# Performance work log

Hardware: AMD Instinct MI355X
Metric: run time of the kernel (lower is better)

## Reference

```python
import jax, jax.numpy as jnp
import numpy as np

B, N, DIM = 32, 577, 768   # N = num_patches + 1
H, DH = 12, 64             # heads, dim_head; inner_dim = H*DH = 768
NEG = -987654321.0         # LSA diagonal mask value from the source


def setup_inputs() -> dict:
    key = jax.random.key(0)
    ks = jax.random.split(key, 5)
    inner = H * DH
    base_scale = DH ** -0.5
    return {
        "x": jax.random.normal(ks[0], (B, N, DIM), dtype=jnp.float32),
        "W_qkv": jax.random.normal(ks[1], (DIM, inner * 3), dtype=jnp.float32) * (DIM ** -0.5),
        "scale": base_scale * (1.0 + 0.01 * jax.random.normal(ks[2], (H,), dtype=jnp.float32)),
        "W_out": jax.random.normal(ks[3], (inner, DIM), dtype=jnp.float32) * (inner ** -0.5),
        "b_out": jnp.zeros((DIM,), dtype=jnp.float32),
    }


def reference(x, W_qkv, scale, W_out, b_out):
    b, n, _ = x.shape
    qkv = x @ W_qkv                                   # [b, n, 3*H*DH]
    q, k, v = jnp.split(qkv, 3, axis=-1)
    to_heads = lambda t: t.reshape(b, n, H, DH).transpose(0, 2, 1, 3)  # b h n d
    q, k, v = to_heads(q), to_heads(k), to_heads(v)
    # per-head learnable scale (LSA)
    dots = jnp.einsum('bhid,bhjd->bhij', q, k) * scale[None, :, None, None]
    # mask self-attention diagonal (eye scatter in the torch source)
    eye = jnp.eye(n, dtype=bool)
    dots = jnp.where(eye[None, None], NEG, dots)
    attn = jax.nn.softmax(dots, axis=-1)
    out = jnp.einsum('bhij,bhjd->bhid', attn, v)      # b h n d
    out = out.transpose(0, 2, 1, 3).reshape(b, n, H * DH)
    return out @ W_out + b_out
```

## Files before the change

kernel.cpp:

```cpp
#include <hip/hip_runtime.h>


typedef _Float16 half8  __attribute__((ext_vector_type(8)));
typedef _Float16 h4f    __attribute__((ext_vector_type(4)));
typedef __fp16   hv2    __attribute__((ext_vector_type(2)));
typedef __fp16   hv4    __attribute__((ext_vector_type(4)));
typedef float    floatx4 __attribute__((ext_vector_type(4)));

#define MTOT   18464
#define NEG_V  (-987654321.0f)
#define VTS    584

__device__ __forceinline__ void gl_lds16(const _Float16* g, _Float16* l) {
    __builtin_amdgcn_global_load_lds(
        (const __attribute__((address_space(1))) unsigned int*)g,
        (__attribute__((address_space(3))) unsigned int*)l,
        16, 0, 0);
}

__global__ __launch_bounds__(256) void cvt_x(const float* __restrict__ x,
                                             _Float16* __restrict__ x16) {
    const size_t idx = ((size_t)blockIdx.x * 256 + threadIdx.x) * 8;
    half8 h = {};
    if (idx < (size_t)MTOT * 768) {
        float4 a = *(const float4*)(x + idx);
        float4 b = *(const float4*)(x + idx + 4);
        h[0] = (_Float16)a.x; h[1] = (_Float16)a.y;
        h[2] = (_Float16)a.z; h[3] = (_Float16)a.w;
        h[4] = (_Float16)b.x; h[5] = (_Float16)b.y;
        h[6] = (_Float16)b.z; h[7] = (_Float16)b.w;
    }
    *(half8*)(x16 + idx) = h;
}

__global__ __launch_bounds__(256) void transpose_w(const float* __restrict__ src,
                                                   _Float16* __restrict__ dst,
                                                   int K, int Ncol) {
    __shared__ float tile[32][33];
    const int n0 = blockIdx.x * 32, k0 = blockIdx.y * 32;
    const int tx = threadIdx.x & 31, ty = threadIdx.x >> 5;
    for (int i = 0; i < 32; i += 8)
        tile[ty + i][tx] = src[(size_t)(k0 + ty + i) * Ncol + (n0 + tx)];
    __syncthreads();
    for (int i = 0; i < 32; i += 8)
        dst[(size_t)(n0 + ty + i) * K + (k0 + tx)] = (_Float16)tile[tx][ty + i];
}

__global__ __launch_bounds__(512, 4) void gemm_qkv(const _Float16* __restrict__ x16,
                                                   const _Float16* __restrict__ wT,
                                                   const float* __restrict__ scale,
                                                   _Float16* __restrict__ qg,
                                                   _Float16* __restrict__ kg,
                                                   _Float16* __restrict__ vT) {
    __shared__ _Float16 As[2][128 * 32];
    __shared__ _Float16 Bs[2][256 * 32];
    const int m0 = blockIdx.x * 128, n0 = blockIdx.y * 256;
    const int tid = threadIdx.x;
    const int lane = tid & 63, wv = tid >> 6;
    const int wrow = wv >> 2, wcol = wv & 3;
    const int lr = lane & 15, lq = lane >> 4;

    const int ra  = tid >> 2,            ca  = (tid & 3) * 8;
    const int rb0 = tid >> 2,            cb0 = (tid & 3) * 8;
    const int rb1 = (512 + tid) >> 2,    cb1 = (tid & 3) * 8;

    floatx4 acc[4][4];
    const floatx4 fz = {0.f, 0.f, 0.f, 0.f};
    for (int i = 0; i < 4; ++i)
        for (int j = 0; j < 4; ++j) acc[i][j] = fz;

    #define STAGE_QKV(ki, bf)                                                     \
        do {                                                                      \
            const int kk_ = (ki) * 32;                                            \
            gl_lds16(x16 + (size_t)(m0 + ra) * 768 + kk_ + ca, &As[bf][wv*64*8]); \
            gl_lds16(wT + (size_t)(n0 + rb0) * 768 + kk_ + cb0, &Bs[bf][wv*64*8]);\
            gl_lds16(wT + (size_t)(n0 + rb1) * 768 + kk_ + cb1,                   \
                     &Bs[bf][(512 + wv*64) * 8]);                                 \
        } while (0)

    STAGE_QKV(0, 0);
    for (int ki = 0; ki < 24; ++ki) {
        const int bf = ki & 1;
        if (ki < 23) {
            STAGE_QKV(ki + 1, bf ^ 1);
            asm volatile("s_waitcnt vmcnt(3)" ::: "memory");
        } else {
            asm volatile("s_waitcnt vmcnt(0)" ::: "memory");
        }
        asm volatile("s_barrier" ::: "memory");

        half8 af[4], bfr[4];
        #pragma unroll
        for (int i = 0; i < 4; ++i)
            af[i] = *(const half8*)&As[bf][(wrow * 64 + i * 16 + lr) * 32 + lq * 8];
        #pragma unroll
        for (int j = 0; j < 4; ++j)
            bfr[j] = *(const half8*)&Bs[bf][(wcol * 64 + j * 16 + lr) * 32 + lq * 8];
        #pragma unroll
        for (int i = 0; i < 4; ++i)
            #pragma unroll
            for (int j = 0; j < 4; ++j)
                acc[i][j] = __builtin_amdgcn_mfma_f32_16x16x32_f16(af[i], bfr[j], acc[i][j], 0, 0, 0);

        asm volatile("s_waitcnt lgkmcnt(0)\n\ts_barrier" ::: "memory");
    }
    #undef STAGE_QKV

    const int cbase = n0 + wcol * 64;
    const int which = cbase / 768;
    const int h = (cbase - which * 768) >> 6;
    const float qsc = (which == 0) ? scale[h] * 1.4426950408889634f : 1.0f;
    #pragma unroll
    for (int j = 0; j < 4; ++j) {
        const int d = j * 16 + lr;
        #pragma unroll
        for (int i = 0; i < 4; ++i)
            #pragma unroll
            for (int r = 0; r < 4; ++r) {
                const int row = m0 + wrow * 64 + i * 16 + lq * 4 + r;
                if (row >= MTOT) continue;
                const unsigned bb = (unsigned)row / 577u;
                const unsigned nn = (unsigned)row - bb * 577u;
                const _Float16 val = (_Float16)(acc[i][j][r] * qsc);
                const size_t head = (size_t)(bb * 12 + h);
                if (which == 0)      qg[(head * 577 + nn) * 64 + d] = val;
                else if (which == 1) kg[(head * 577 + nn) * 64 + d] = val;
                else                 vT[(head * 64 + d) * VTS + nn] = val;
            }
    }
}

__global__ __launch_bounds__(256) void attn_kernel(const _Float16* __restrict__ qg,
                                                   const _Float16* __restrict__ kg,
                                                   const _Float16* __restrict__ vT,
                                                   _Float16* __restrict__ Og) {
    __shared__ __align__(16) _Float16 Ks[64 * 64];
    __shared__ __align__(16) _Float16 Vs[64 * 64];
    const int qt = blockIdx.x, h = blockIdx.y, b = blockIdx.z;
    const int tid = threadIdx.x, lane = tid & 63, wv = tid >> 6;
    const int lr = lane & 15, lq = lane >> 4;
    const size_t head = (size_t)(b * 12 + h);
    const _Float16* qh = qg + head * 577 * 64;
    const _Float16* kh = kg + head * 577 * 64;
    const _Float16* vh = vT + head * 64 * VTS;
    const int q0 = qt * 128;
    const int xs = lq ^ (lr & 7), xs4 = xs ^ 4;

    half8 bq[2][2];
    #pragma unroll
    for (int st = 0; st < 2; ++st) {
        const int qi = q0 + st * 64 + wv * 16 + lr;
        const int qc = qi < 577 ? qi : 576;
        bq[st][0] = *(const half8*)(qh + (size_t)qc * 64 + lq * 8);
        bq[st][1] = *(const half8*)(qh + (size_t)qc * 64 + 32 + lq * 8);
    }

    const floatx4 fz = {0.f, 0.f, 0.f, 0.f};
    floatx4 ot[2][4];
    #pragma unroll
    for (int st = 0; st < 2; ++st)
        #pragma unroll
        for (int c = 0; c < 4; ++c) ot[st][c] = fz;
    float sacc[2] = {0.f, 0.f};

    for (int kt = 0; kt < 10; ++kt) {
        const int j0 = kt * 64;
        __syncthreads();
        #pragma unroll
        for (int t = 0; t < 2; ++t) {
            const int c = t * 256 + wv * 64 + lane;
            const int row = c >> 3, cl = (c & 7) ^ (row & 7);
            gl_lds16(kh + (size_t)(j0 + row) * 64 + cl * 8,
                     Ks + (t * 256 + wv * 64) * 8);
            gl_lds16(vh + (size_t)row * VTS + j0 + cl * 8,
                     Vs + (t * 256 + wv * 64) * 8);
        }
        __syncthreads();

        half8 ak[4][2];
        #pragma unroll
        for (int ct = 0; ct < 4; ++ct) {
            const int base = (ct * 16 + lr) * 64;
            ak[ct][0] = *(const half8*)&Ks[base + xs * 8];
            ak[ct][1] = *(const half8*)&Ks[base + xs4 * 8];
        }

        floatx4 s[2][4];
        #pragma unroll
        for (int st = 0; st < 2; ++st)
            #pragma unroll
            for (int ct = 0; ct < 4; ++ct) {
                floatx4 t = __builtin_amdgcn_mfma_f32_16x16x32_f16(ak[ct][0], bq[st][0], fz, 0, 0, 0);
                s[st][ct] = __builtin_amdgcn_mfma_f32_16x16x32_f16(ak[ct][1], bq[st][1], t, 0, 0, 0);
            }

        if (kt == 9) {
            #pragma unroll
            for (int st = 0; st < 2; ++st) {
                s[st][0][0] = (lq == 0) ? s[st][0][0] : -INFINITY;
                s[st][0][1] = -INFINITY; s[st][0][2] = -INFINITY; s[st][0][3] = -INFINITY;
                #pragma unroll
                for (int ct = 1; ct < 4; ++ct) {
                    s[st][ct][0] = -INFINITY; s[st][ct][1] = -INFINITY;
                    s[st][ct][2] = -INFINITY; s[st][ct][3] = -INFINITY;
                }
            }
        }
        #pragma unroll
        for (int st = 0; st < 2; ++st) {
            if (kt == qt * 2 + st) {
                #pragma unroll
                for (int ct = 0; ct < 4; ++ct)
                    if (ct == wv) {
                        #pragma unroll
                        for (int r = 0; r < 4; ++r)
                            if (lq * 4 + r == lr) s[st][ct][r] = -INFINITY;
                    }
            }
        }

        hv4 pk[2][4];
        #pragma unroll
        for (int st = 0; st < 2; ++st)
            #pragma unroll
            for (int ct = 0; ct < 4; ++ct) {
                const float p0 = __builtin_amdgcn_exp2f(s[st][ct][0]);
                const float p1 = __builtin_amdgcn_exp2f(s[st][ct][1]);
                const float p2 = __builtin_amdgcn_exp2f(s[st][ct][2]);
                const float p3 = __builtin_amdgcn_exp2f(s[st][ct][3]);
                sacc[st] += (p0 + p1) + (p2 + p3);
                const hv2 lo = __builtin_amdgcn_cvt_pkrtz(p0, p1);
                const hv2 hi = __builtin_amdgcn_cvt_pkrtz(p2, p3);
                pk[st][ct] = __builtin_shufflevector(lo, hi, 0, 1, 2, 3);
            }

        #pragma unroll
        for (int jc = 0; jc < 4; ++jc) {
            const int csv = ((jc << 1) | (lq >> 1)) ^ (lr & 7);
            #pragma unroll
            for (int ctd = 0; ctd < 4; ++ctd) {
                const hv4 av = *(const hv4*)&Vs[(ctd * 16 + lr) * 64 + csv * 8 + (lq & 1) * 4];
                #pragma unroll
                for (int st = 0; st < 2; ++st)
                    ot[st][ctd] = __builtin_amdgcn_mfma_f32_16x16x16f16(av, pk[st][jc], ot[st][ctd], 0, 0, 0);
            }
        }
    }

    #pragma unroll
    for (int st = 0; st < 2; ++st) {
        float l = sacc[st];
        l += __shfl_xor(l, 16, 64);
        l += __shfl_xor(l, 32, 64);
        const float linv = 1.f / l;
        const int i = q0 + st * 64 + wv * 16 + lr;
        if (i < 577) {
            #pragma unroll
            for (int ctd = 0; ctd < 4; ++ctd) {
                h4f ov;
                #pragma unroll
                for (int r = 0; r < 4; ++r) ov[r] = (_Float16)(ot[st][ctd][r] * linv);
                *(h4f*)(Og + ((size_t)(b * 577 + i)) * 768 + h * 64 + ctd * 16 + lq * 4) = ov;
            }
        }
    }
}

__global__ __launch_bounds__(512, 4) void gemm_out(const _Float16* __restrict__ Og,
                                                   const _Float16* __restrict__ wT,
                                                   const float* __restrict__ bias,
                                                   float* __restrict__ out) {
    __shared__ _Float16 As[2][128 * 32];
    __shared__ _Float16 Bs[2][256 * 32];
    const int m0 = blockIdx.x * 128, n0 = blockIdx.y * 256;
    const int tid = threadIdx.x;
    const int lane = tid & 63, wv = tid >> 6;
    const int wrow = wv >> 2, wcol = wv & 3;
    const int lr = lane & 15, lq = lane >> 4;

    const int ra  = tid >> 2,         ca  = (tid & 3) * 8;
    const int rb0 = tid >> 2,         cb0 = (tid & 3) * 8;
    const int rb1 = (512 + tid) >> 2, cb1 = (tid & 3) * 8;

    floatx4 acc[4][4];
    const floatx4 fz = {0.f, 0.f, 0.f, 0.f};
    for (int i = 0; i < 4; ++i)
        for (int j = 0; j < 4; ++j) acc[i][j] = fz;

    #define STAGE_OUT(ki, bf)                                                     \
        do {                                                                      \
            const int kk_ = (ki) * 32;                                            \
            gl_lds16(Og + (size_t)(m0 + ra) * 768 + kk_ + ca, &As[bf][wv*64*8]);  \
            gl_lds16(wT + (size_t)(n0 + rb0) * 768 + kk_ + cb0, &Bs[bf][wv*64*8]);\
            gl_lds16(wT + (size_t)(n0 + rb1) * 768 + kk_ + cb1,                   \
                     &Bs[bf][(512 + wv*64) * 8]);                                 \
        } while (0)

    STAGE_OUT(0, 0);
    for (int ki = 0; ki < 24; ++ki) {
        const int bf = ki & 1;
        if (ki < 23) {
            STAGE_OUT(ki + 1, bf ^ 1);
            asm volatile("s_waitcnt vmcnt(3)" ::: "memory");
        } else {
            asm volatile("s_waitcnt vmcnt(0)" ::: "memory");
        }
        asm volatile("s_barrier" ::: "memory");

        half8 af[4], bfr[4];
        #pragma unroll
        for (int i = 0; i < 4; ++i)
            af[i] = *(const half8*)&As[bf][(wrow * 64 + i * 16 + lr) * 32 + lq * 8];
        #pragma unroll
        for (int j = 0; j < 4; ++j)
            bfr[j] = *(const half8*)&Bs[bf][(wcol * 64 + j * 16 + lr) * 32 + lq * 8];
        #pragma unroll
        for (int i = 0; i < 4; ++i)
            #pragma unroll
            for (int j = 0; j < 4; ++j)
                acc[i][j] = __builtin_amdgcn_mfma_f32_16x16x32_f16(af[i], bfr[j], acc[i][j], 0, 0, 0);

        asm volatile("s_waitcnt lgkmcnt(0)\n\ts_barrier" ::: "memory");
    }
    #undef STAGE_OUT

    #pragma unroll
    for (int j = 0; j < 4; ++j) {
        const int c = n0 + wcol * 64 + j * 16 + lr;
        const float bv = bias[c];
        #pragma unroll
        for (int i = 0; i < 4; ++i)
            #pragma unroll
            for (int r = 0; r < 4; ++r) {
                const int row = m0 + wrow * 64 + i * 16 + lq * 4 + r;
                if (row < MTOT) out[(size_t)row * 768 + c] = acc[i][j][r] + bv;
            }
    }
}

extern "C" void kernel_launch(void* const* d_in, const int* in_sizes, int n_in,
                              void* d_out, int out_size, void* d_ws, size_t ws_size,
                              hipStream_t stream) {
    const float* x      = (const float*)d_in[0];
    const float* W_qkv  = (const float*)d_in[1];
    const float* scale  = (const float*)d_in[2];
    const float* W_out  = (const float*)d_in[3];
    const float* b_out  = (const float*)d_in[4];
    float* out = (float*)d_out;

    char* ws = (char*)d_ws;
    _Float16* x16   = (_Float16*)(ws);
    _Float16* Og    = x16;
    _Float16* qg    = (_Float16*)(ws + 28508160u);
    _Float16* kg    = (_Float16*)(ws + 28508160u + 28360704u);
    _Float16* vT    = (_Float16*)(ws + 28508160u + 2u * 28360704u);
    _Float16* WqkvT = (_Float16*)(ws + 28508160u + 2u * 28360704u + 28704768u);
    _Float16* WoutT = WqkvT + (size_t)2304 * 768;

    cvt_x<<<6960, 256, 0, stream>>>(x, x16);
    transpose_w<<<dim3(72, 24), 256, 0, stream>>>(W_qkv, WqkvT, 768, 2304);
    transpose_w<<<dim3(24, 24), 256, 0, stream>>>(W_out, WoutT, 768, 768);
    gemm_qkv<<<dim3(145, 9), 512, 0, stream>>>(x16, WqkvT, scale, qg, kg, vT);
    attn_kernel<<<dim3(5, 12, 32), 256, 0, stream>>>(qg, kg, vT, Og);
    gemm_out<<<dim3(145, 3), 512, 0, stream>>>(Og, WoutT, b_out, out);
}
```

Baseline: 352.1 us.

## Deepen GEMM pipelines to six LDS stages, swizzle tiles, double-buffer attention K/V

Both projection GEMMs now use a 6-slot LDS ring with loads issued four k-steps ahead, and drop the trailing barrier because the ring distance keeps reuse safe. LDS tile columns are XOR-swizzled to reduce bank conflicts, and s_setprio brackets the MFMA blocks. The attention kernel double-buffers K/V tiles so the next tile's loads overlap the current compute. The larger LDS footprint lowers the occupancy target to 2 blocks per CU, which trades latency hiding from extra resident waves for deeper prefetch.

After: 404.1 us. 14.8% more time.

```diff
diff --git a/kernel.cpp b/kernel.cpp
--- a/kernel.cpp
+++ b/kernel.cpp
@@ -46,43 +46,51 @@
         dst[(size_t)(n0 + ty + i) * K + (k0 + tx)] = (_Float16)tile[tx][ty + i];
 }
 
-__global__ __launch_bounds__(512, 4) void gemm_qkv(const _Float16* __restrict__ x16,
+__global__ __launch_bounds__(512, 2) void gemm_qkv(const _Float16* __restrict__ x16,
                                                    const _Float16* __restrict__ wT,
                                                    const float* __restrict__ scale,
                                                    _Float16* __restrict__ qg,
                                                    _Float16* __restrict__ kg,
                                                    _Float16* __restrict__ vT) {
-    __shared__ _Float16 As[2][128 * 32];
-    __shared__ _Float16 Bs[2][256 * 32];
+    __shared__ _Float16 As[6][128 * 32];
+    __shared__ _Float16 Bs[6][256 * 32];
     const int m0 = blockIdx.x * 128, n0 = blockIdx.y * 256;
     const int tid = threadIdx.x;
     const int lane = tid & 63, wv = tid >> 6;
     const int wrow = wv >> 2, wcol = wv & 3;
     const int lr = lane & 15, lq = lane >> 4;
 
-    const int ra  = tid >> 2,            ca  = (tid & 3) * 8;
-    const int rb0 = tid >> 2,            cb0 = (tid & 3) * 8;
-    const int rb1 = (512 + tid) >> 2,    cb1 = (tid & 3) * 8;
+    const int ra  = tid >> 2,         ca  = (((tid & 3) ^ ((ra  >> 1) & 3)) * 8);
+    const int rb0 = tid >> 2,         cb0 = (((tid & 3) ^ ((rb0 >> 1) & 3)) * 8);
+    const int rb1 = (512 + tid) >> 2, cb1 = (((tid & 3) ^ ((rb1 >> 1) & 3)) * 8);
+    const int xc = (lq ^ ((lr >> 1) & 3)) * 8;
 
     floatx4 acc[4][4];
     const floatx4 fz = {0.f, 0.f, 0.f, 0.f};
     for (int i = 0; i < 4; ++i)
         for (int j = 0; j < 4; ++j) acc[i][j] = fz;
 
-    #define STAGE_QKV(ki, bf)                                                     \
-        do {                                                                      \
-            const int kk_ = (ki) * 32;                                            \
-            gl_lds16(x16 + (size_t)(m0 + ra) * 768 + kk_ + ca, &As[bf][wv*64*8]); \
-            gl_lds16(wT + (size_t)(n0 + rb0) * 768 + kk_ + cb0, &Bs[bf][wv*64*8]);\
-            gl_lds16(wT + (size_t)(n0 + rb1) * 768 + kk_ + cb1,                   \
-                     &Bs[bf][(512 + wv*64) * 8]);                                 \
+    #define STAGE_QKV(ki_, bfx)                                                    \
+        do {                                                                       \
+            const int kk_ = (ki_) * 32;                                            \
+            gl_lds16(x16 + (size_t)(m0 + ra) * 768 + kk_ + ca, &As[bfx][wv*64*8]); \
+            gl_lds16(wT + (size_t)(n0 + rb0) * 768 + kk_ + cb0, &Bs[bfx][wv*64*8]);\
+            gl_lds16(wT + (size_t)(n0 + rb1) * 768 + kk_ + cb1,                    \
+                     &Bs[bfx][(512 + wv*64) * 8]);                                 \
         } while (0)
 
-    STAGE_QKV(0, 0);
+    STAGE_QKV(0, 0); STAGE_QKV(1, 1); STAGE_QKV(2, 2); STAGE_QKV(3, 3);
+    int bf = 0, sf = 4;
     for (int ki = 0; ki < 24; ++ki) {
-        const int bf = ki & 1;
-        if (ki < 23) {
-            STAGE_QKV(ki + 1, bf ^ 1);
+        if (ki < 20) {
+            STAGE_QKV(ki + 4, sf);
+            sf = (sf == 5) ? 0 : sf + 1;
+            asm volatile("s_waitcnt vmcnt(12)" ::: "memory");
+        } else if (ki == 20) {
+            asm volatile("s_waitcnt vmcnt(9)" ::: "memory");
+        } else if (ki == 21) {
+            asm volatile("s_waitcnt vmcnt(6)" ::: "memory");
+        } else if (ki == 22) {
             asm volatile("s_waitcnt vmcnt(3)" ::: "memory");
         } else {
             asm volatile("s_waitcnt vmcnt(0)" ::: "memory");
@@ -92,17 +100,18 @@
         half8 af[4], bfr[4];
         #pragma unroll
         for (int i = 0; i < 4; ++i)
-            af[i] = *(const half8*)&As[bf][(wrow * 64 + i * 16 + lr) * 32 + lq * 8];
+            af[i] = *(const half8*)&As[bf][(wrow * 64 + i * 16 + lr) * 32 + xc];
         #pragma unroll
         for (int j = 0; j < 4; ++j)
-            bfr[j] = *(const half8*)&Bs[bf][(wcol * 64 + j * 16 + lr) * 32 + lq * 8];
+            bfr[j] = *(const half8*)&Bs[bf][(wcol * 64 + j * 16 + lr) * 32 + xc];
+        __builtin_amdgcn_s_setprio(1);
         #pragma unroll
         for (int i = 0; i < 4; ++i)
             #pragma unroll
             for (int j = 0; j < 4; ++j)
                 acc[i][j] = __builtin_amdgcn_mfma_f32_16x16x32_f16(af[i], bfr[j], acc[i][j], 0, 0, 0);
-
-        asm volatile("s_waitcnt lgkmcnt(0)\n\ts_barrier" ::: "memory");
+        __builtin_amdgcn_s_setprio(0);
+        bf = (bf == 5) ? 0 : bf + 1;
     }
     #undef STAGE_QKV
 
@@ -134,8 +143,8 @@
                                                    const _Float16* __restrict__ kg,
                                                    const _Float16* __restrict__ vT,
                                                    _Float16* __restrict__ Og) {
-    __shared__ __align__(16) _Float16 Ks[64 * 64];
-    __shared__ __align__(16) _Float16 Vs[64 * 64];
+    __shared__ __align__(16) _Float16 Ks[2][64 * 64];
+    __shared__ __align__(16) _Float16 Vs[2][64 * 64];
     const int qt = blockIdx.x, h = blockIdx.y, b = blockIdx.z;
     const int tid = threadIdx.x, lane = tid & 63, wv = tid >> 6;
     const int lr = lane & 15, lq = lane >> 4;
@@ -155,6 +164,23 @@
         bq[st][1] = *(const half8*)(qh + (size_t)qc * 64 + 32 + lq * 8);
     }
 
+    #define PREF(kt_, pb_)                                               \
+        do {                                                             \
+            const int j0_ = (kt_) * 64;                                  \
+            {   const int c_ = wv * 64 + lane;                           \
+                const int r_ = c_ >> 3, cl_ = (c_ & 7) ^ (r_ & 7);       \
+                gl_lds16(kh + (size_t)(j0_ + r_) * 64 + cl_ * 8,         \
+                         &Ks[pb_][(wv * 64) * 8]);                       \
+                gl_lds16(vh + (size_t)r_ * VTS + j0_ + cl_ * 8,          \
+                         &Vs[pb_][(wv * 64) * 8]);   }                   \
+            {   const int c_ = 256 + wv * 64 + lane;                     \
+                const int r_ = c_ >> 3, cl_ = (c_ & 7) ^ (r_ & 7);       \
+                gl_lds16(kh + (size_t)(j0_ + r_) * 64 + cl_ * 8,         \
+                         &Ks[pb_][(256 + wv * 64) * 8]);                 \
+                gl_lds16(vh + (size_t)r_ * VTS + j0_ + cl_ * 8,          \
+                         &Vs[pb_][(256 + wv * 64) * 8]);   }             \
+        } while (0)
+
     const floatx4 fz = {0.f, 0.f, 0.f, 0.f};
     floatx4 ot[2][4];
     #pragma unroll
@@ -163,29 +189,27 @@
         for (int c = 0; c < 4; ++c) ot[st][c] = fz;
     float sacc[2] = {0.f, 0.f};
 
+    PREF(0, 0);
     for (int kt = 0; kt < 10; ++kt) {
-        const int j0 = kt * 64;
-        __syncthreads();
-        #pragma unroll
-        for (int t = 0; t < 2; ++t) {
-            const int c = t * 256 + wv * 64 + lane;
-            const int row = c >> 3, cl = (c & 7) ^ (row & 7);
-            gl_lds16(kh + (size_t)(j0 + row) * 64 + cl * 8,
-                     Ks + (t * 256 + wv * 64) * 8);
-            gl_lds16(vh + (size_t)row * VTS + j0 + cl * 8,
-                     Vs + (t * 256 + wv * 64) * 8);
-        }
-        __syncthreads();
+        const int bf = kt & 1;
+        if (kt < 9) {
+            PREF(kt + 1, bf ^ 1);
+            asm volatile("s_waitcnt vmcnt(4)" ::: "memory");
+        } else {
+            asm volatile("s_waitcnt vmcnt(0)" ::: "memory");
+        }
+        asm volatile("s_barrier" ::: "memory");
 
         half8 ak[4][2];
         #pragma unroll
         for (int ct = 0; ct < 4; ++ct) {
             const int base = (ct * 16 + lr) * 64;
-            ak[ct][0] = *(const half8*)&Ks[base + xs * 8];
-            ak[ct][1] = *(const half8*)&Ks[base + xs4 * 8];
+            ak[ct][0] = *(const half8*)&Ks[bf][base + xs * 8];
+            ak[ct][1] = *(const half8*)&Ks[bf][base + xs4 * 8];
         }
 
         floatx4 s[2][4];
+        __builtin_amdgcn_s_setprio(1);
         #pragma unroll
         for (int st = 0; st < 2; ++st)
             #pragma unroll
@@ -193,6 +217,7 @@
                 floatx4 t = __builtin_amdgcn_mfma_f32_16x16x32_f16(ak[ct][0], bq[st][0], fz, 0, 0, 0);
                 s[st][ct] = __builtin_amdgcn_mfma_f32_16x16x32_f16(ak[ct][1], bq[st][1], t, 0, 0, 0);
             }
+        __builtin_amdgcn_s_setprio(0);
 
         if (kt == 9) {
             #pragma unroll
@@ -234,18 +259,23 @@
                 pk[st][ct] = __builtin_shufflevector(lo, hi, 0, 1, 2, 3);
             }
 
+        __builtin_amdgcn_s_setprio(1);
         #pragma unroll
         for (int jc = 0; jc < 4; ++jc) {
             const int csv = ((jc << 1) | (lq >> 1)) ^ (lr & 7);
             #pragma unroll
             for (int ctd = 0; ctd < 4; ++ctd) {
-                const hv4 av = *(const hv4*)&Vs[(ctd * 16 + lr) * 64 + csv * 8 + (lq & 1) * 4];
+                const hv4 av = *(const hv4*)&Vs[bf][(ctd * 16 + lr) * 64 + csv * 8 + (lq & 1) * 4];
                 #pragma unroll
                 for (int st = 0; st < 2; ++st)
                     ot[st][ctd] = __builtin_amdgcn_mfma_f32_16x16x16f16(av, pk[st][jc], ot[st][ctd], 0, 0, 0);
             }
         }
-    }
+        __builtin_amdgcn_s_setprio(0);
+
+        asm volatile("s_waitcnt lgkmcnt(0)\n\ts_barrier" ::: "memory");
+    }
+    #undef PREF
 
     #pragma unroll
     for (int st = 0; st < 2; ++st) {
@@ -266,41 +296,49 @@
     }
 }
 
-__global__ __launch_bounds__(512, 4) void gemm_out(const _Float16* __restrict__ Og,
+__global__ __launch_bounds__(512, 2) void gemm_out(const _Float16* __restrict__ Og,
                                                    const _Float16* __restrict__ wT,
                                                    const float* __restrict__ bias,
                                                    float* __restrict__ out) {
-    __shared__ _Float16 As[2][128 * 32];
-    __shared__ _Float16 Bs[2][256 * 32];
+    __shared__ _Float16 As[6][128 * 32];
+    __shared__ _Float16 Bs[6][256 * 32];
     const int m0 = blockIdx.x * 128, n0 = blockIdx.y * 256;
     const int tid = threadIdx.x;
     const int lane = tid & 63, wv = tid >> 6;
     const int wrow = wv >> 2, wcol = wv & 3;
     const int lr = lane & 15, lq = lane >> 4;
 
-    const int ra  = tid >> 2,         ca  = (tid & 3) * 8;
-    const int rb0 = tid >> 2,         cb0 = (tid & 3) * 8;
-    const int rb1 = (512 + tid) >> 2, cb1 = (tid & 3) * 8;
+    const int ra  = tid >> 2,         ca  = (((tid & 3) ^ ((ra  >> 1) & 3)) * 8);
+    const int rb0 = tid >> 2,         cb0 = (((tid & 3) ^ ((rb0 >> 1) & 3)) * 8);
+    const int rb1 = (512 + tid) >> 2, cb1 = (((tid & 3) ^ ((rb1 >> 1) & 3)) * 8);
+    const int xc = (lq ^ ((lr >> 1) & 3)) * 8;
 
     floatx4 acc[4][4];
     const floatx4 fz = {0.f, 0.f, 0.f, 0.f};
     for (int i = 0; i < 4; ++i)
         for (int j = 0; j < 4; ++j) acc[i][j] = fz;
 
-    #define STAGE_OUT(ki, bf)                                                     \
-        do {                                                                      \
-            const int kk_ = (ki) * 32;                                            \
-            gl_lds16(Og + (size_t)(m0 + ra) * 768 + kk_ + ca, &As[bf][wv*64*8]);  \
-            gl_lds16(wT + (size_t)(n0 + rb0) * 768 + kk_ + cb0, &Bs[bf][wv*64*8]);\
-            gl_lds16(wT + (size_t)(n0 + rb1) * 768 + kk_ + cb1,                   \
-                     &Bs[bf][(512 + wv*64) * 8]);                                 \
+    #define STAGE_OUT(ki_, bfx)                                                    \
+        do {                                                                       \
+            const int kk_ = (ki_) * 32;                                            \
+            gl_lds16(Og + (size_t)(m0 + ra) * 768 + kk_ + ca, &As[bfx][wv*64*8]);  \
+            gl_lds16(wT + (size_t)(n0 + rb0) * 768 + kk_ + cb0, &Bs[bfx][wv*64*8]);\
+            gl_lds16(wT + (size_t)(n0 + rb1) * 768 + kk_ + cb1,                    \
+                     &Bs[bfx][(512 + wv*64) * 8]);                                 \
         } while (0)
 
-    STAGE_OUT(0, 0);
+    STAGE_OUT(0, 0); STAGE_OUT(1, 1); STAGE_OUT(2, 2); STAGE_OUT(3, 3);
+    int bf = 0, sf = 4;
     for (int ki = 0; ki < 24; ++ki) {
-        const int bf = ki & 1;
-        if (ki < 23) {
-            STAGE_OUT(ki + 1, bf ^ 1);
+        if (ki < 20) {
+            STAGE_OUT(ki + 4, sf);
+            sf = (sf == 5) ? 0 : sf + 1;
+            asm volatile("s_waitcnt vmcnt(12)" ::: "memory");
+        } else if (ki == 20) {
+            asm volatile("s_waitcnt vmcnt(9)" ::: "memory");
+        } else if (ki == 21) {
+            asm volatile("s_waitcnt vmcnt(6)" ::: "memory");
+        } else if (ki == 22) {
             asm volatile("s_waitcnt vmcnt(3)" ::: "memory");
         } else {
             asm volatile("s_waitcnt vmcnt(0)" ::: "memory");
@@ -310,17 +348,18 @@
         half8 af[4], bfr[4];
         #pragma unroll
         for (int i = 0; i < 4; ++i)
-            af[i] = *(const half8*)&As[bf][(wrow * 64 + i * 16 + lr) * 32 + lq * 8];
+            af[i] = *(const half8*)&As[bf][(wrow * 64 + i * 16 + lr) * 32 + xc];
         #pragma unroll
         for (int j = 0; j < 4; ++j)
-            bfr[j] = *(const half8*)&Bs[bf][(wcol * 64 + j * 16 + lr) * 32 + lq * 8];
+            bfr[j] = *(const half8*)&Bs[bf][(wcol * 64 + j * 16 + lr) * 32 + xc];
+        __builtin_amdgcn_s_setprio(1);
         #pragma unroll
         for (int i = 0; i < 4; ++i)
             #pragma unroll
             for (int j = 0; j < 4; ++j)
                 acc[i][j] = __builtin_amdgcn_mfma_f32_16x16x32_f16(af[i], bfr[j], acc[i][j], 0, 0, 0);
-
-        asm volatile("s_waitcnt lgkmcnt(0)\n\ts_barrier" ::: "memory");
+        __builtin_amdgcn_s_setprio(0);
+        bf = (bf == 5) ? 0 : bf + 1;
     }
     #undef STAGE_OUT
 
```
